# Optimization experiments

Hardware: AMD Instinct MI355X
Metric: run time of the kernel (lower is better)

The kernel has to match this reference:

```python
import jax, jax.numpy as jnp
import numpy as np

B, N, T, D = 4, 1000, 12, 64
HID, EF = 128, 64
E = 64000
STEP = 0.1

def setup_inputs() -> dict:
    key = jax.random.key(0)
    ks = jax.random.split(key, 16)
    s = 0.05
    return {
        'x': jax.random.normal(ks[0], (B, N, T, D), dtype=jnp.float32),
        'batch_idx': jax.random.randint(ks[1], (E,), 0, B, dtype=jnp.int32),
        'sender_idx': jax.random.randint(ks[2], (E,), 0, N, dtype=jnp.int32),
        'receiver_idx': jax.random.randint(ks[3], (E,), 0, N, dtype=jnp.int32),
        'A1_w': jax.random.normal(ks[4], (D, HID), dtype=jnp.float32) * s,
        'A1_b': jax.random.normal(ks[5], (HID,), dtype=jnp.float32) * s,
        'A2_w': jax.random.normal(ks[6], (D, HID), dtype=jnp.float32) * s,
        'A2_b': jax.random.normal(ks[7], (HID,), dtype=jnp.float32) * s,
        'A3_w': jax.random.normal(ks[8], (HID, EF), dtype=jnp.float32) * s,
        'A3_b': jax.random.normal(ks[9], (EF,), dtype=jnp.float32) * s,
        'A4_w': jax.random.normal(ks[10], (EF, D), dtype=jnp.float32) * s,
        'A4_b': jax.random.normal(ks[11], (D,), dtype=jnp.float32) * s,
    }

def reference(x, batch_idx, sender_idx, receiver_idx,
              A1_w, A1_b, A2_w, A2_b, A3_w, A3_b, A4_w, A4_b):
    # x: [B, N, T, D]; edge list gathers (equivalent to adj.nonzero)
    x_sender = x[batch_idx, sender_idx]      # [E, T, D]
    x_receiver = x[batch_idx, receiver_idx]  # [E, T, D]

    def edge_mlp(a, b):
        # A3(relu(A1(a) + A2(b))), applied per edge-time element
        h = jax.nn.relu(a @ A1_w + A1_b + b @ A2_w + A2_b)
        return h @ A3_w + A3_b

    z_ij = edge_mlp(x_sender, x_receiver)
    z_ji = edge_mlp(x_receiver, x_sender)
    v_ij_pre = jax.nn.relu(z_ij - z_ji) @ A4_w + A4_b  # [E, T, D]

    seg_send = batch_idx * N + sender_idx  # [E]
    # numerically-stable segment softmax over outgoing edges of each sender
    max_logits = jax.ops.segment_max(v_ij_pre, seg_send, num_segments=B * N)
    exp_centered = jnp.exp(v_ij_pre - max_logits[seg_send])
    denom = jax.ops.segment_sum(exp_centered, seg_send, num_segments=B * N)
    v_ij = exp_centered / (denom[seg_send] + 1e-12)  # [E, T, D]

    messages = v_ij * x_sender
    seg_recv = batch_idx * N + receiver_idx
    inbound = jax.ops.segment_sum(messages, seg_recv, num_segments=B * N)
    inbound = inbound.reshape(B, N, T, D)

    x_updated = x + STEP * (inbound - x)
    return x_updated, v_ij
```

## Files before the change

### kernel.cpp

```cpp
#include <hip/hip_runtime.h>
#include <math.h>

#define BB 4
#define NN 1000
#define TT 12
#define DD 64
#define HIDN 128
#define EFN 64
#define EE 64000
#define BN (BB*NN)
#define ROWS (BN*TT)
#define TD (TT*DD)
#define STEPF 0.1f
#define MAXSEG 27

typedef _Float16 f16x8 __attribute__((ext_vector_type(8)));
typedef float f32x4 __attribute__((ext_vector_type(4)));

__device__ __forceinline__ unsigned short f2h(float x) {
    _Float16 h = (_Float16)x;
    return __builtin_bit_cast(unsigned short, h);
}
__device__ __forceinline__ float h2f(unsigned short u) {
    return (float)__builtin_bit_cast(_Float16, u);
}

__global__ __launch_bounds__(256) void k_zero(int* __restrict__ p, int n) {
    int i = blockIdx.x * 256 + threadIdx.x;
    if (i < n) p[i] = 0;
}

__global__ __launch_bounds__(256) void k_count(const int* __restrict__ bi,
                                               const int* __restrict__ si,
                                               const int* __restrict__ ri,
                                               int* __restrict__ cnt_s,
                                               int* __restrict__ cnt_r) {
    int e = blockIdx.x * 256 + threadIdx.x;
    if (e < EE) {
        int b = bi[e];
        atomicAdd(&cnt_s[b * NN + si[e]], 1);
        atomicAdd(&cnt_r[b * NN + ri[e]], 1);
    }
}

__global__ __launch_bounds__(256) void k_scan(const int* __restrict__ cnt_s,
                                              const int* __restrict__ cnt_r,
                                              int* __restrict__ rp_s, int* __restrict__ rp_r,
                                              int* __restrict__ cur_s, int* __restrict__ cur_r) {
    const int* cnt = blockIdx.x ? cnt_r : cnt_s;
    int* rp  = blockIdx.x ? rp_r  : rp_s;
    int* cur = blockIdx.x ? cur_r : cur_s;
    __shared__ int part[256];
    int tid = threadIdx.x;
    const int chunk = 16;
    int bgn = tid * chunk;
    int end = min(bgn + chunk, BN);
    int s = 0;
    for (int i = bgn; i < end; ++i) s += cnt[i];
    part[tid] = s;
    __syncthreads();
    for (int off = 1; off < 256; off <<= 1) {
        int v = part[tid];
        if (tid >= off) v += part[tid - off];
        __syncthreads();
        part[tid] = v;
        __syncthreads();
    }
    int run = tid ? part[tid - 1] : 0;
    for (int i = bgn; i < end; ++i) { rp[i] = run; cur[i] = run; run += cnt[i]; }
    if (tid == 255) rp[BN] = part[255];
}

__global__ __launch_bounds__(256) void k_fill(const int* __restrict__ bi,
                                              const int* __restrict__ si,
                                              const int* __restrict__ ri,
                                              int* __restrict__ cur_s, int* __restrict__ cur_r,
                                              int* __restrict__ el_s, int* __restrict__ el_r) {
    int e = blockIdx.x * 256 + threadIdx.x;
    if (e < EE) {
        int b = bi[e];
        int ps = atomicAdd(&cur_s[b * NN + si[e]], 1);
        el_s[ps] = e;
        int pr = atomicAdd(&cur_r[b * NN + ri[e]], 1);
        el_r[pr] = e;
    }
}

__global__ __launch_bounds__(256) void k_prep_w(const float* __restrict__ A3_w,
                                                const float* __restrict__ A4_w,
                                                unsigned short* __restrict__ W3f,
                                                unsigned short* __restrict__ W4f) {
    int i = blockIdx.x * 256 + threadIdx.x;
    if (i < 8192) {
        int j = i & 7, lane = (i >> 3) & 63, nt = (i >> 9) & 3, kt = i >> 11;
        int k = kt * 32 + (lane >> 4) * 8 + j;
        int n = nt * 16 + (lane & 15);
        W3f[i] = f2h(A3_w[k * 64 + n]);
    } else if (i < 12288) {
        int ii = i - 8192;
        int j = ii & 7, lane = (ii >> 3) & 63, nt = (ii >> 9) & 3, kt = ii >> 11;
        int k = kt * 32 + (lane >> 4) * 8 + j;
        int n = nt * 16 + (lane & 15);
        W4f[ii] = f2h(A4_w[k * 64 + n]);
    }
}

__global__ __launch_bounds__(256) void k_node_proj(const float* __restrict__ x,
                                                   const float* __restrict__ A1_w,
                                                   const float* __restrict__ A1_b,
                                                   const float* __restrict__ A2_w,
                                                   const float* __restrict__ A2_b,
                                                   unsigned short* __restrict__ Q1,
                                                   unsigned short* __restrict__ Q2) {
    __shared__ float xs[16][64];
    int tid = threadIdx.x;
    int row0 = blockIdx.x * 16;
    {
        int i = tid * 4;
        int r = i >> 6, k = i & 63;
        *(float4*)&xs[r][k] = *(const float4*)&x[(size_t)(row0 + r) * 64 + k];
    }
    __syncthreads();
    int h = tid & 127;
    int w = tid >> 7;
    const float* W = w ? A2_w : A1_w;
    float bias = w ? A2_b[h] : A1_b[h];
    float acc[16];
#pragma unroll
    for (int r = 0; r < 16; ++r) acc[r] = 0.f;
    for (int k = 0; k < 64; ++k) {
        float wv = W[k * 128 + h];
#pragma unroll
        for (int r = 0; r < 16; ++r) acc[r] += xs[r][k] * wv;
    }
    unsigned short* Qo = w ? Q2 : Q1;
    for (int r = 0; r < 16; ++r) Qo[(size_t)(row0 + r) * 128 + h] = f2h(acc[r] + bias);
}

__global__ __launch_bounds__(256, 3) void k_edge_seg(const unsigned short* __restrict__ Q1,
                                                     const unsigned short* __restrict__ Q2,
                                                     const int* __restrict__ ri,
                                                     const int* __restrict__ rp_s,
                                                     const int* __restrict__ el_s,
                                                     const unsigned short* __restrict__ W3f,
                                                     const unsigned short* __restrict__ W4f,
                                                     const float* __restrict__ A4_b,
                                                     float* __restrict__ v) {
    __shared__ unsigned short Vseg[MAXSEG][12][68];
    __shared__ __align__(16) _Float16 Hs[4][16][72];

    int seg = blockIdx.x;
    int beg = rp_s[seg], end = rp_s[seg + 1];
    int S = end - beg;
    if (S == 0) return;

    int tid  = threadIdx.x;
    int lane = tid & 63;
    int wv   = tid >> 6;
    int quad = lane >> 4;
    int m    = lane & 15;
    int kbase = quad * 8;
    int b    = seg / NN;

    f16x8 w3[4][4], w4[2][4];
#pragma unroll
    for (int kt = 0; kt < 4; ++kt)
#pragma unroll
        for (int nt = 0; nt < 4; ++nt)
            w3[kt][nt] = *(const f16x8*)&W3f[((kt * 4 + nt) * 64 + lane) * 8];
#pragma unroll
    for (int kt = 0; kt < 2; ++kt)
#pragma unroll
        for (int nt = 0; nt < 4; ++nt)
            w4[kt][nt] = *(const f16x8*)&W4f[((kt * 4 + nt) * 64 + lane) * 8];
    float b4[4];
#pragma unroll
    for (int nt = 0; nt < 4; ++nt) b4[nt] = A4_b[nt * 16 + m];

    const f16x8 hz = {0, 0, 0, 0, 0, 0, 0, 0};

    const unsigned short* ps1 = Q1 + (size_t)seg * (TT * HIDN) + m * 128 + kbase;
    const unsigned short* ps2 = Q2 + (size_t)seg * (TT * HIDN) + m * 128 + kbase;

    for (int li = wv; li < S; li += 4) {
        int e = el_s[beg + li];
        int rn = b * NN + ri[e];

        f16x8 g[4];
        if (m < 12) {
            const unsigned short* pr1 = Q1 + (size_t)rn * (TT * HIDN) + m * 128 + kbase;
            const unsigned short* pr2 = Q2 + (size_t)rn * (TT * HIDN) + m * 128 + kbase;
            f16x8 s1[4], s2[4], r1[4], r2[4];
#pragma unroll
            for (int kt = 0; kt < 4; ++kt) {
                s1[kt] = *(const f16x8*)(ps1 + kt * 32);
                r2[kt] = *(const f16x8*)(pr2 + kt * 32);
                r1[kt] = *(const f16x8*)(pr1 + kt * 32);
                s2[kt] = *(const f16x8*)(ps2 + kt * 32);
            }
#pragma unroll
            for (int kt = 0; kt < 4; ++kt) {
                f16x8 a = s1[kt] + r2[kt];
                f16x8 c = r1[kt] + s2[kt];
                g[kt] = __builtin_elementwise_max(a, hz)
                      - __builtin_elementwise_max(c, hz);
            }
        } else {
#pragma unroll
            for (int kt = 0; kt < 4; ++kt) g[kt] = hz;
        }

        f32x4 acc[4];
#pragma unroll
        for (int nt = 0; nt < 4; ++nt) acc[nt] = (f32x4){0.f, 0.f, 0.f, 0.f};
#pragma unroll
        for (int kt = 0; kt < 4; ++kt)
#pragma unroll
            for (int nt = 0; nt < 4; ++nt)
                acc[nt] = __builtin_amdgcn_mfma_f32_16x16x32_f16(g[kt], w3[kt][nt], acc[nt], 0, 0, 0);

#pragma unroll
        for (int nt = 0; nt < 4; ++nt)
#pragma unroll
            for (int r = 0; r < 4; ++r)
                Hs[wv][quad * 4 + r][nt * 16 + m] = (_Float16)fmaxf(acc[nt][r], 0.f);

        const _Float16* hp = &Hs[wv][m][kbase];
        f16x8 hf0 = *(const f16x8*)hp;
        f16x8 hf1 = *(const f16x8*)(hp + 32);

#pragma unroll
        for (int nt = 0; nt < 4; ++nt) {
            f32x4 o = (f32x4){b4[nt], b4[nt], b4[nt], b4[nt]};
            o = __builtin_amdgcn_mfma_f32_16x16x32_f16(hf0, w4[0][nt], o, 0, 0, 0);
            o = __builtin_amdgcn_mfma_f32_16x16x32_f16(hf1, w4[1][nt], o, 0, 0, 0);
            if (quad < 3) {
                if (li < MAXSEG) {
#pragma unroll
                    for (int r = 0; r < 4; ++r)
                        Vseg[li][quad * 4 + r][nt * 16 + m] = f2h(o[r]);
                } else {
                    size_t ebase = (size_t)e * TD;
#pragma unroll
                    for (int r = 0; r < 4; ++r)
                        v[ebase + (quad * 4 + r) * 64 + nt * 16 + m] = o[r];
                }
            }
        }
    }
    __syncthreads();

    int d  = tid & 63;
    int tb = tid >> 6;
    int nL = min(S, MAXSEG);

    float mj[3] = {-1e30f, -1e30f, -1e30f};
    for (int i = 0; i < nL; ++i) {
#pragma unroll
        for (int jj = 0; jj < 3; ++jj)
            mj[jj] = fmaxf(mj[jj], h2f(Vseg[i][tb + 4 * jj][d]));
    }
    for (int i = MAXSEG; i < S; ++i) {
        size_t ebase = (size_t)el_s[beg + i] * TD;
#pragma unroll
        for (int jj = 0; jj < 3; ++jj)
            mj[jj] = fmaxf(mj[jj], v[ebase + (tb + 4 * jj) * 64 + d]);
    }

    float sj[3] = {0.f, 0.f, 0.f};
    for (int i = 0; i < nL; ++i) {
#pragma unroll
        for (int jj = 0; jj < 3; ++jj)
            sj[jj] += __expf(h2f(Vseg[i][tb + 4 * jj][d]) - mj[jj]);
    }
    for (int i = MAXSEG; i < S; ++i) {
        size_t ebase = (size_t)el_s[beg + i] * TD;
#pragma unroll
        for (int jj = 0; jj < 3; ++jj)
            sj[jj] += __expf(v[ebase + (tb + 4 * jj) * 64 + d] - mj[jj]);
    }

    float inv[3];
#pragma unroll
    for (int jj = 0; jj < 3; ++jj) inv[jj] = 1.f / (sj[jj] + 1e-12f);

    for (int i = 0; i < nL; ++i) {
        size_t ebase = (size_t)el_s[beg + i] * TD;
#pragma unroll
        for (int jj = 0; jj < 3; ++jj)
            v[ebase + (tb + 4 * jj) * 64 + d] =
                __expf(h2f(Vseg[i][tb + 4 * jj][d]) - mj[jj]) * inv[jj];
    }
    for (int i = MAXSEG; i < S; ++i) {
        size_t ebase = (size_t)el_s[beg + i] * TD;
#pragma unroll
        for (int jj = 0; jj < 3; ++jj) {
            size_t a = ebase + (tb + 4 * jj) * 64 + d;
            v[a] = __expf(v[a] - mj[jj]) * inv[jj];
        }
    }
}

__global__ __launch_bounds__(256) void k_aggregate(const int* __restrict__ rp_r,
                                                   const int* __restrict__ el_r,
                                                   const int* __restrict__ si,
                                                   const float* __restrict__ x,
                                                   const float* __restrict__ v,
                                                   float* __restrict__ xout) {
    int node = blockIdx.x;
    int beg = rp_r[node], end = rp_r[node + 1];
    int tid = threadIdx.x;
    int b = node / NN;
    __shared__ int e_l[256];
    __shared__ int sb_l[256];
    float acc[3] = {0.f, 0.f, 0.f};
    for (int c = beg; c < end; c += 256) {
        int cnt = min(end - c, 256);
        if (tid < cnt) {
            int e = el_r[c + tid];
            e_l[tid] = e;
            sb_l[tid] = (b * NN + si[e]) * TD;
        }
        __syncthreads();
        for (int i = 0; i < cnt; ++i) {
            size_t vb = (size_t)e_l[i] * TD;
            int sb = sb_l[i];
#pragma unroll
            for (int jj = 0; jj < 3; ++jj) {
                int j = tid + jj * 256;
                acc[jj] += v[vb + j] * x[sb + j];
            }
        }
        __syncthreads();
    }
    size_t nb = (size_t)node * TD;
#pragma unroll
    for (int jj = 0; jj < 3; ++jj) {
        int j = tid + jj * 256;
        float xv = x[nb + j];
        xout[nb + j] = xv + STEPF * (acc[jj] - xv);
    }
}

extern "C" void kernel_launch(void* const* d_in, const int* in_sizes, int n_in,
                              void* d_out, int out_size, void* d_ws, size_t ws_size,
                              hipStream_t stream) {
    const float* x    = (const float*)d_in[0];
    const int*   bi   = (const int*)d_in[1];
    const int*   si   = (const int*)d_in[2];
    const int*   ri   = (const int*)d_in[3];
    const float* A1_w = (const float*)d_in[4];
    const float* A1_b = (const float*)d_in[5];
    const float* A2_w = (const float*)d_in[6];
    const float* A2_b = (const float*)d_in[7];
    const float* A3_w = (const float*)d_in[8];
    const float* A4_w = (const float*)d_in[10];
    const float* A4_b = (const float*)d_in[11];

    float* xout = (float*)d_out;
    float* v    = (float*)d_out + (size_t)BN * TD;

    unsigned short* Q1  = (unsigned short*)d_ws;
    unsigned short* Q2  = Q1 + (size_t)ROWS * HIDN;
    unsigned short* W3f = Q2 + (size_t)ROWS * HIDN;
    unsigned short* W4f = W3f + 8192;
    int* cnt_s = (int*)(W4f + 4096);
    int* cnt_r = cnt_s + BN;
    int* rp_s  = cnt_r + BN;
    int* rp_r  = rp_s + BN + 1;
    int* cur_s = rp_r + BN + 1;
    int* cur_r = cur_s + BN;
    int* el_s  = cur_r + BN;
    int* el_r  = el_s + EE;

    k_zero<<<(2 * BN + 255) / 256, 256, 0, stream>>>(cnt_s, 2 * BN);
    k_count<<<EE / 256, 256, 0, stream>>>(bi, si, ri, cnt_s, cnt_r);
    k_scan<<<2, 256, 0, stream>>>(cnt_s, cnt_r, rp_s, rp_r, cur_s, cur_r);
    k_fill<<<EE / 256, 256, 0, stream>>>(bi, si, ri, cur_s, cur_r, el_s, el_r);
    k_prep_w<<<48, 256, 0, stream>>>(A3_w, A4_w, W3f, W4f);
    k_node_proj<<<ROWS / 16, 256, 0, stream>>>(x, A1_w, A1_b, A2_w, A2_b, Q1, Q2);
    k_edge_seg<<<BN, 256, 0, stream>>>(Q1, Q2, ri, rp_s, el_s, W3f, W4f, A4_b, v);
    k_aggregate<<<BN, 256, 0, stream>>>(rp_r, el_r, si, x, v, xout);
}
```

Baseline: 533.5 us.

## Stage W4 and edge indices in LDS, hoist sender rows, swizzle Vseg

Moves the W4 weight fragments from registers into shared memory and loads the sender Q1/Q2 rows once per block instead of once per edge. Edge and receiver indices for the first 48 edges are prefetched into LDS. The gather/MFMA loop is interleaved per k-tile to shorten register live ranges, and the Vseg buffer loses its padding in favour of an XOR swizzle, with MAXSEG reduced to fit LDS. The aim is lower register pressure and fewer redundant global loads. The cost is more LDS traffic, and more edges spill to the slower global-memory path for segments longer than 22.

```diff
diff --git a/kernel.cpp b/kernel.cpp
--- a/kernel.cpp
+++ b/kernel.cpp
@@ -12,7 +12,8 @@
 #define ROWS (BN*TT)
 #define TD (TT*DD)
 #define STEPF 0.1f
-#define MAXSEG 27
+#define MAXSEG 22
+#define ELDS 48
 
 typedef _Float16 f16x8 __attribute__((ext_vector_type(8)));
 typedef float f32x4 __attribute__((ext_vector_type(4)));
@@ -137,17 +138,21 @@
     for (int r = 0; r < 16; ++r) Qo[(size_t)(row0 + r) * 128 + h] = f2h(acc[r] + bias);
 }
 
-__global__ __launch_bounds__(256, 3) void k_edge_seg(const unsigned short* __restrict__ Q1,
-                                                     const unsigned short* __restrict__ Q2,
-                                                     const int* __restrict__ ri,
-                                                     const int* __restrict__ rp_s,
-                                                     const int* __restrict__ el_s,
-                                                     const unsigned short* __restrict__ W3f,
-                                                     const unsigned short* __restrict__ W4f,
-                                                     const float* __restrict__ A4_b,
-                                                     float* __restrict__ v) {
-    __shared__ unsigned short Vseg[MAXSEG][12][68];
+__global__ __launch_bounds__(256) __attribute__((amdgpu_waves_per_eu(3, 3)))
+void k_edge_seg(const unsigned short* __restrict__ Q1,
+                const unsigned short* __restrict__ Q2,
+                const int* __restrict__ ri,
+                const int* __restrict__ rp_s,
+                const int* __restrict__ el_s,
+                const unsigned short* __restrict__ W3f,
+                const unsigned short* __restrict__ W4f,
+                const float* __restrict__ A4_b,
+                float* __restrict__ v) {
+    __shared__ unsigned short Vseg[MAXSEG][12][64];
     __shared__ __align__(16) _Float16 Hs[4][16][72];
+    __shared__ __align__(16) _Float16 W4s[4096];
+    __shared__ int e_lds[ELDS];
+    __shared__ int rn_lds[ELDS];
 
     int seg = blockIdx.x;
     int beg = rp_s[seg], end = rp_s[seg + 1];
@@ -162,62 +167,70 @@
     int kbase = quad * 8;
     int b    = seg / NN;
 
-    f16x8 w3[4][4], w4[2][4];
+    for (int i = tid; i < 512; i += 256)
+        *(f16x8*)&W4s[i * 8] = *(const f16x8*)(const void*)&W4f[i * 8];
+    if (tid < ELDS && tid < S) {
+        int e = el_s[beg + tid];
+        e_lds[tid] = e;
+        rn_lds[tid] = b * NN + ri[e];
+    }
+
+    f16x8 w3[4][4];
 #pragma unroll
     for (int kt = 0; kt < 4; ++kt)
 #pragma unroll
         for (int nt = 0; nt < 4; ++nt)
-            w3[kt][nt] = *(const f16x8*)&W3f[((kt * 4 + nt) * 64 + lane) * 8];
-#pragma unroll
-    for (int kt = 0; kt < 2; ++kt)
-#pragma unroll
-        for (int nt = 0; nt < 4; ++nt)
-            w4[kt][nt] = *(const f16x8*)&W4f[((kt * 4 + nt) * 64 + lane) * 8];
+            w3[kt][nt] = *(const f16x8*)(const void*)&W3f[((kt * 4 + nt) * 64 + lane) * 8];
     float b4[4];
 #pragma unroll
     for (int nt = 0; nt < 4; ++nt) b4[nt] = A4_b[nt * 16 + m];
 
     const f16x8 hz = {0, 0, 0, 0, 0, 0, 0, 0};
 
-    const unsigned short* ps1 = Q1 + (size_t)seg * (TT * HIDN) + m * 128 + kbase;
-    const unsigned short* ps2 = Q2 + (size_t)seg * (TT * HIDN) + m * 128 + kbase;
+    f16x8 s1[4], s2[4];
+    if (m < 12) {
+        const unsigned short* p1 = Q1 + (size_t)seg * (TT * HIDN) + m * 128 + kbase;
+        const unsigned short* p2 = Q2 + (size_t)seg * (TT * HIDN) + m * 128 + kbase;
+#pragma unroll
+        for (int kt = 0; kt < 4; ++kt) {
+            s1[kt] = *(const f16x8*)(const void*)(p1 + kt * 32);
+            s2[kt] = *(const f16x8*)(const void*)(p2 + kt * 32);
+        }
+    } else {
+#pragma unroll
+        for (int kt = 0; kt < 4; ++kt) { s1[kt] = hz; s2[kt] = hz; }
+    }
+
+    __syncthreads();
 
     for (int li = wv; li < S; li += 4) {
-        int e = el_s[beg + li];
-        int rn = b * NN + ri[e];
-
-        f16x8 g[4];
-        if (m < 12) {
-            const unsigned short* pr1 = Q1 + (size_t)rn * (TT * HIDN) + m * 128 + kbase;
-            const unsigned short* pr2 = Q2 + (size_t)rn * (TT * HIDN) + m * 128 + kbase;
-            f16x8 s1[4], s2[4], r1[4], r2[4];
-#pragma unroll
-            for (int kt = 0; kt < 4; ++kt) {
-                s1[kt] = *(const f16x8*)(ps1 + kt * 32);
-                r2[kt] = *(const f16x8*)(pr2 + kt * 32);
-                r1[kt] = *(const f16x8*)(pr1 + kt * 32);
-                s2[kt] = *(const f16x8*)(ps2 + kt * 32);
+        int e, rn;
+        if (li < ELDS) { e = e_lds[li]; rn = rn_lds[li]; }
+        else           { e = el_s[beg + li]; rn = b * NN + ri[e]; }
+
+        const unsigned short* pr1 = Q1 + (size_t)rn * (TT * HIDN) + m * 128 + kbase;
+        const unsigned short* pr2 = Q2 + (size_t)rn * (TT * HIDN) + m * 128 + kbase;
+
+        f32x4 acc[4];
+#pragma unroll
+        for (int nt = 0; nt < 4; ++nt) acc[nt] = (f32x4){0.f, 0.f, 0.f, 0.f};
+#pragma unroll
+        for (int kt = 0; kt < 4; ++kt) {
+            f16x8 g;
+            if (m < 12) {
+                f16x8 r1 = *(const f16x8*)(const void*)(pr1 + kt * 32);
+                f16x8 r2 = *(const f16x8*)(const void*)(pr2 + kt * 32);
+                f16x8 a = s1[kt] + r2;
+                f16x8 c = r1 + s2[kt];
+                g = __builtin_elementwise_max(a, hz)
+                  - __builtin_elementwise_max(c, hz);
+            } else {
+                g = hz;
             }
 #pragma unroll
-            for (int kt = 0; kt < 4; ++kt) {
-                f16x8 a = s1[kt] + r2[kt];
-                f16x8 c = r1[kt] + s2[kt];
-                g[kt] = __builtin_elementwise_max(a, hz)
-                      - __builtin_elementwise_max(c, hz);
-            }
-        } else {
-#pragma unroll
-            for (int kt = 0; kt < 4; ++kt) g[kt] = hz;
-        }
-
-        f32x4 acc[4];
-#pragma unroll
-        for (int nt = 0; nt < 4; ++nt) acc[nt] = (f32x4){0.f, 0.f, 0.f, 0.f};
-#pragma unroll
-        for (int kt = 0; kt < 4; ++kt)
-#pragma unroll
             for (int nt = 0; nt < 4; ++nt)
-                acc[nt] = __builtin_amdgcn_mfma_f32_16x16x32_f16(g[kt], w3[kt][nt], acc[nt], 0, 0, 0);
+                acc[nt] = __builtin_amdgcn_mfma_f32_16x16x32_f16(g, w3[kt][nt], acc[nt], 0, 0, 0);
+        }
 
 #pragma unroll
         for (int nt = 0; nt < 4; ++nt)
@@ -232,13 +245,14 @@
 #pragma unroll
         for (int nt = 0; nt < 4; ++nt) {
             f32x4 o = (f32x4){b4[nt], b4[nt], b4[nt], b4[nt]};
-            o = __builtin_amdgcn_mfma_f32_16x16x32_f16(hf0, w4[0][nt], o, 0, 0, 0);
-            o = __builtin_amdgcn_mfma_f32_16x16x32_f16(hf1, w4[1][nt], o, 0, 0, 0);
+            o = __builtin_amdgcn_mfma_f32_16x16x32_f16(hf0, *(const f16x8*)&W4s[(nt * 64 + lane) * 8], o, 0, 0, 0);
+            o = __builtin_amdgcn_mfma_f32_16x16x32_f16(hf1, *(const f16x8*)&W4s[((4 + nt) * 64 + lane) * 8], o, 0, 0, 0);
             if (quad < 3) {
                 if (li < MAXSEG) {
+                    int cc = ((nt ^ quad) << 4) | m;
 #pragma unroll
                     for (int r = 0; r < 4; ++r)
-                        Vseg[li][quad * 4 + r][nt * 16 + m] = f2h(o[r]);
+                        Vseg[li][quad * 4 + r][cc] = f2h(o[r]);
                 } else {
                     size_t ebase = (size_t)e * TD;
 #pragma unroll
@@ -253,15 +267,19 @@
     int d  = tid & 63;
     int tb = tid >> 6;
     int nL = min(S, MAXSEG);
+    int dd[3];
+#pragma unroll
+    for (int jj = 0; jj < 3; ++jj) dd[jj] = d ^ (jj << 4);
 
     float mj[3] = {-1e30f, -1e30f, -1e30f};
     for (int i = 0; i < nL; ++i) {
 #pragma unroll
         for (int jj = 0; jj < 3; ++jj)
-            mj[jj] = fmaxf(mj[jj], h2f(Vseg[i][tb + 4 * jj][d]));
+            mj[jj] = fmaxf(mj[jj], h2f(Vseg[i][tb + 4 * jj][dd[jj]]));
     }
     for (int i = MAXSEG; i < S; ++i) {
-        size_t ebase = (size_t)el_s[beg + i] * TD;
+        int e = (i < ELDS) ? e_lds[i] : el_s[beg + i];
+        size_t ebase = (size_t)e * TD;
 #pragma unroll
         for (int jj = 0; jj < 3; ++jj)
             mj[jj] = fmaxf(mj[jj], v[ebase + (tb + 4 * jj) * 64 + d]);
@@ -271,10 +289,11 @@
     for (int i = 0; i < nL; ++i) {
 #pragma unroll
         for (int jj = 0; jj < 3; ++jj)
-            sj[jj] += __expf(h2f(Vseg[i][tb + 4 * jj][d]) - mj[jj]);
+            sj[jj] += __expf(h2f(Vseg[i][tb + 4 * jj][dd[jj]]) - mj[jj]);
     }
     for (int i = MAXSEG; i < S; ++i) {
-        size_t ebase = (size_t)el_s[beg + i] * TD;
+        int e = (i < ELDS) ? e_lds[i] : el_s[beg + i];
+        size_t ebase = (size_t)e * TD;
 #pragma unroll
         for (int jj = 0; jj < 3; ++jj)
             sj[jj] += __expf(v[ebase + (tb + 4 * jj) * 64 + d] - mj[jj]);
@@ -285,14 +304,16 @@
     for (int jj = 0; jj < 3; ++jj) inv[jj] = 1.f / (sj[jj] + 1e-12f);
 
     for (int i = 0; i < nL; ++i) {
-        size_t ebase = (size_t)el_s[beg + i] * TD;
+        int e = (i < ELDS) ? e_lds[i] : el_s[beg + i];
+        size_t ebase = (size_t)e * TD;
 #pragma unroll
         for (int jj = 0; jj < 3; ++jj)
             v[ebase + (tb + 4 * jj) * 64 + d] =
-                __expf(h2f(Vseg[i][tb + 4 * jj][d]) - mj[jj]) * inv[jj];
+                __expf(h2f(Vseg[i][tb + 4 * jj][dd[jj]]) - mj[jj]) * inv[jj];
     }
     for (int i = MAXSEG; i < S; ++i) {
-        size_t ebase = (size_t)el_s[beg + i] * TD;
+        int e = (i < ELDS) ? e_lds[i] : el_s[beg + i];
+        size_t ebase = (size_t)e * TD;
 #pragma unroll
         for (int jj = 0; jj < 3; ++jj) {
             size_t a = ebase + (tb + 4 * jj) * 64 + d;
```

Measured after the change: 514.5 us. 1.04x faster.
